# Optimization experiments

Measured on AMD Instinct MI355X. Metric: run time of the kernel, lower is better.

Reference implementation:

```python
import jax, jax.numpy as jnp
import numpy as np

H, KV, D, WIN = 16, 4, 128, 1024


def _rope(x, cos, sin):
    # x: [B, H, S, D]; cos/sin: [1, 1, S, D//2]
    d = x.shape[-1] // 2
    x1, x2 = x[..., :d], x[..., d:]
    S = x.shape[2]
    c, s = cos[:, :, :S], sin[:, :, :S]
    return jnp.concatenate([x1 * c + x2 * s, -x1 * s + x2 * c], axis=-1)


def _rms_norm(x):
    eps = jnp.finfo(x.dtype).eps
    return x * jax.lax.rsqrt(jnp.mean(jnp.square(x), axis=-1, keepdims=True) + eps)


def setup_inputs() -> dict:
    key = jax.random.key(0)
    ks = jax.random.split(key, 7)
    B, S, E = 2, 2048, 2048
    return {
        "x": jax.random.normal(ks[0], (B, S, E), jnp.float32),
        "cos": jax.random.normal(ks[1], (1, 1, S, D // 2), jnp.float32),
        "sin": jax.random.normal(ks[2], (1, 1, S, D // 2), jnp.float32),
        "Wq": jax.random.normal(ks[3], (H * D, E), jnp.float32) * 0.02,
        "Wk": jax.random.normal(ks[4], (KV * D, E), jnp.float32) * 0.02,
        "Wv": jax.random.normal(ks[5], (KV * D, E), jnp.float32) * 0.02,
        "Wo": jax.random.normal(ks[6], (E, H * D), jnp.float32) * 0.02,
    }


def reference(x, cos, sin, Wq, Wk, Wv, Wo):
    B, S, E = x.shape
    rep = H // KV
    # projections -> [B, heads, S, D]
    q = (x @ Wq.T).reshape(B, S, H, D).transpose(0, 2, 1, 3)
    k = (x @ Wk.T).reshape(B, S, KV, D).transpose(0, 2, 1, 3)
    v = (x @ Wv.T).reshape(B, S, KV, D).transpose(0, 2, 1, 3)
    # GQA: materialize repeated K/V heads (matches repeat_interleave)
    k = jnp.repeat(k, rep, axis=1)
    v = jnp.repeat(v, rep, axis=1)
    # RoPE then QK RMSNorm (no learned scale)
    q = _rms_norm(_rope(q, cos, sin))
    k = _rms_norm(_rope(k, cos, sin))
    scores = jnp.einsum("bhqd,bhkd->bhqk", q, k) * (D ** -0.5)
    # causal & sliding-window mask
    i = jnp.arange(S)[:, None]
    j = jnp.arange(S)[None, :]
    mask = (i >= j) & (jnp.abs(i - j) < WIN)
    scores = jnp.where(mask[None, None], scores, -jnp.inf)
    attn = jax.nn.softmax(scores, axis=-1)
    out = jnp.einsum("bhqk,bhkd->bhqd", attn, v)
    out = out.transpose(0, 2, 1, 3).reshape(B, S, H * D)
    return out @ Wo.T
```

## Files before the change

kernel.cpp:

```cpp
#include <hip/hip_runtime.h>
#include <stdint.h>

using bf16 = __bf16;
typedef __bf16 bf16x8 __attribute__((ext_vector_type(8)));
typedef __bf16 bf16x4 __attribute__((ext_vector_type(4)));
typedef float f32x4 __attribute__((ext_vector_type(4)));

#define H_ 16
#define KV_ 4
#define D_ 128
#define WIN_ 1024
#define B_ 2
#define S_ 2048
#define E_ 2048
#define HD_ 2048

__device__ __forceinline__ void gld_lds16(const void* gptr, void* lptr) {
    __builtin_amdgcn_global_load_lds(
        (__attribute__((address_space(1))) void*)(uintptr_t)gptr,
        (__attribute__((address_space(3))) void*)(uintptr_t)lptr, 16, 0, 0);
}

__global__ __launch_bounds__(256) void cvt_all(const float* __restrict__ x,
                                               const float* __restrict__ wq,
                                               const float* __restrict__ wk,
                                               const float* __restrict__ wv,
                                               const float* __restrict__ wo,
                                               bf16* __restrict__ dst) {
    int i = (blockIdx.x * 256 + threadIdx.x) * 4;
    const float* src;
    int off;
    if (i < 8388608)       { src = x;  off = 0; }
    else if (i < 12582912) { src = wq; off = 8388608; }
    else if (i < 13631488) { src = wk; off = 12582912; }
    else if (i < 14680064) { src = wv; off = 13631488; }
    else                   { src = wo; off = 14680064; }
    const float4 v = *(const float4*)(src + (i - off));
    bf16x4 o = {(bf16)v.x, (bf16)v.y, (bf16)v.z, (bf16)v.w};
    *(bf16x4*)(dst + i) = o;
}


template <typename OutT>
__global__ __launch_bounds__(256) void gemm_bt(const bf16* __restrict__ A,
                                               const bf16* __restrict__ W,
                                               OutT* __restrict__ C, int K, int ldc) {
    __shared__ alignas(16) bf16 As[128 * 64];
    __shared__ alignas(16) bf16 Bs[128 * 64];
    const int t = threadIdx.x;
    const int lane = t & 63;
    const int wave = t >> 6;
    const int l15 = lane & 15;
    const int quad = lane >> 4;
    const int fsw = l15 & 7;
    const int wm = (wave & 1) * 64;
    const int wn = (wave >> 1) * 64;
    const int m0 = blockIdx.x * 128;
    const int n0 = blockIdx.y * 128;

    f32x4 acc[4][4] = {};

    const int sr = t >> 3;
    const int su = ((t & 7) ^ ((t >> 3) & 7)) * 8;
    const bf16* Ap = A + (size_t)(m0 + sr) * K + su;
    const bf16* Wp = W + (size_t)(n0 + sr) * K + su;

    for (int k0 = 0; k0 < K; k0 += 64) {
#pragma unroll
        for (int c = 0; c < 4; ++c) {
            gld_lds16(Ap + k0 + (size_t)c * 32 * K, &As[c * 2048 + t * 8]);
            gld_lds16(Wp + k0 + (size_t)c * 32 * K, &Bs[c * 2048 + t * 8]);
        }
        __syncthreads();
#pragma unroll
        for (int kh = 0; kh < 2; ++kh) {
            bf16x8 af[4], bfr[4];
#pragma unroll
            for (int i = 0; i < 4; ++i) {
                af[i] = *(const bf16x8*)&As[(wm + i * 16 + l15) * 64 +
                                            (((kh * 4 + quad) ^ fsw) * 8)];
                bfr[i] = *(const bf16x8*)&Bs[(wn + i * 16 + l15) * 64 +
                                             (((kh * 4 + quad) ^ fsw) * 8)];
            }
#pragma unroll
            for (int i = 0; i < 4; ++i)
#pragma unroll
                for (int j = 0; j < 4; ++j)
                    acc[i][j] =
                        __builtin_amdgcn_mfma_f32_16x16x32_bf16(af[i], bfr[j], acc[i][j], 0, 0, 0);
        }
        __syncthreads();
    }
#pragma unroll
    for (int i = 0; i < 4; ++i) {
        const int row = m0 + wm + i * 16 + quad * 4;
#pragma unroll
        for (int j = 0; j < 4; ++j) {
            const int col = n0 + wn + j * 16 + l15;
#pragma unroll
            for (int r = 0; r < 4; ++r) C[(size_t)(row + r) * ldc + col] = (OutT)acc[i][j][r];
        }
    }
}

__global__ __launch_bounds__(256) void gemm_qkv_rope(const bf16* __restrict__ A,
                                                     const bf16* __restrict__ W,
                                                     const float* __restrict__ cosp,
                                                     const float* __restrict__ sinp,
                                                     bf16* __restrict__ qn,
                                                     bf16* __restrict__ kn,
                                                     bf16* __restrict__ vt) {
    __shared__ alignas(16) unsigned char smem[128 * 136 * 2];
    bf16* As = (bf16*)smem;
    bf16* Bs = (bf16*)(smem + 16384);
    bf16* Cs = (bf16*)smem;
    const int t = threadIdx.x;
    const int lane = t & 63;
    const int wave = t >> 6;
    const int l15 = lane & 15;
    const int quad = lane >> 4;
    const int fsw = l15 & 7;
    const int wm = (wave & 1) * 64;
    const int wn = (wave >> 1) * 64;
    const int m0 = blockIdx.x * 128;
    const int n0 = blockIdx.y * 128;
    const int K = E_;

    f32x4 acc[4][4] = {};

    const int sr = t >> 3;
    const int su = ((t & 7) ^ ((t >> 3) & 7)) * 8;
    const bf16* Ap = A + (size_t)(m0 + sr) * K + su;
    const bf16* Wp = W + (size_t)(n0 + sr) * K + su;

    for (int k0 = 0; k0 < K; k0 += 64) {
#pragma unroll
        for (int c = 0; c < 4; ++c) {
            gld_lds16(Ap + k0 + (size_t)c * 32 * K, &As[c * 2048 + t * 8]);
            gld_lds16(Wp + k0 + (size_t)c * 32 * K, &Bs[c * 2048 + t * 8]);
        }
        __syncthreads();
#pragma unroll
        for (int kh = 0; kh < 2; ++kh) {
            bf16x8 af[4], bfr[4];
#pragma unroll
            for (int i = 0; i < 4; ++i) {
                af[i] = *(const bf16x8*)&As[(wm + i * 16 + l15) * 64 +
                                            (((kh * 4 + quad) ^ fsw) * 8)];
                bfr[i] = *(const bf16x8*)&Bs[(wn + i * 16 + l15) * 64 +
                                             (((kh * 4 + quad) ^ fsw) * 8)];
            }
#pragma unroll
            for (int i = 0; i < 4; ++i)
#pragma unroll
                for (int j = 0; j < 4; ++j)
                    acc[i][j] =
                        __builtin_amdgcn_mfma_f32_16x16x32_bf16(af[i], bfr[j], acc[i][j], 0, 0, 0);
        }
        __syncthreads();
    }

#pragma unroll
    for (int i = 0; i < 4; ++i) {
        const int row = wm + i * 16 + quad * 4;
#pragma unroll
        for (int j = 0; j < 4; ++j) {
            const int col = wn + j * 16 + l15;
#pragma unroll
            for (int r = 0; r < 4; ++r) Cs[(row + r) * 136 + col] = (bf16)acc[i][j][r];
        }
    }
    __syncthreads();

    const int unit = n0 >> 7;
    if (unit < 20) {
        const int row = t >> 1;
        const int half = t & 1;
        const int gr = m0 + row;
        const int bb = gr >> 11;
        const int s = gr & 2047;
        const bf16* crow = &Cs[row * 136 + half * 32];
        const float* cp = cosp + s * 64 + half * 32;
        const float* sp = sinp + s * 64 + half * 32;
        bf16x8 xa[4], xb2[4];
#pragma unroll
        for (int u = 0; u < 4; ++u) {
            xa[u] = *(const bf16x8*)(crow + u * 8);
            xb2[u] = *(const bf16x8*)(crow + 64 + u * 8);
        }
        float y1[32], y2[32], ss = 0.0f;
#pragma unroll
        for (int u = 0; u < 4; ++u)
#pragma unroll
            for (int e = 0; e < 8; ++e) {
                const int jj = u * 8 + e;
                const float x1 = (float)xa[u][e];
                const float x2 = (float)xb2[u][e];
                const float c = cp[jj];
                const float sn = sp[jj];
                y1[jj] = x1 * c + x2 * sn;
                y2[jj] = x2 * c - x1 * sn;
                ss += y1[jj] * y1[jj] + y2[jj] * y2[jj];
            }
        ss += __shfl_xor(ss, 1, 64);
        float rr = rsqrtf(ss * (1.0f / 128.0f) + 1.1920929e-7f);
        bf16* dst;
        if (unit < 16) {
            rr *= 0.12751740f;
            dst = qn + ((size_t)(bb * H_ + unit) * S_ + s) * 128 + half * 32;
        } else {
            dst = kn + ((size_t)(bb * KV_ + (unit - 16)) * S_ + s) * 128 + half * 32;
        }
#pragma unroll
        for (int u = 0; u < 4; ++u) {
            bf16x8 p1, p2;
#pragma unroll
            for (int e = 0; e < 8; ++e) {
                p1[e] = (bf16)(y1[u * 8 + e] * rr);
                p2[e] = (bf16)(y2[u * 8 + e] * rr);
            }
            *(bf16x8*)(dst + u * 8) = p1;
            *(bf16x8*)(dst + 64 + u * 8) = p2;
        }
    } else {
        const int jv = unit - 20;
        const int d = t >> 1;
        const int sl0 = (t & 1) * 64;
        const int s0 = (m0 & 2047) + sl0;
        const int bb = m0 >> 11;
        bf16* vdst = vt + ((size_t)(bb * KV_ + jv) * 128 + d) * S_ + s0;
#pragma unroll
        for (int u = 0; u < 8; ++u) {
            bf16x8 pk;
#pragma unroll
            for (int e = 0; e < 8; ++e) pk[e] = Cs[(sl0 + u * 8 + e) * 136 + d];
            *(bf16x8*)(vdst + u * 8) = pk;
        }
    }
}

__global__ __launch_bounds__(256, 4) void attn_fwd(const bf16* __restrict__ Qn,
                                                   const bf16* __restrict__ Kn,
                                                   const bf16* __restrict__ Vt,
                                                   bf16* __restrict__ Out) {
    __shared__ alignas(16) bf16 Ks[64 * 128];
    __shared__ alignas(16) bf16 Vs[128 * 64];
    __shared__ alignas(16) bf16 Ps[4 * 16 * 64];

    const int t = threadIdx.x;
    const int lane = t & 63;
    const int wave = t >> 6;
    const int l15 = lane & 15;
    const int quad = lane >> 4;
    const int swz = l15 & 7;
    const int qb0 = blockIdx.x * 64;
    const int h = blockIdx.y;
    const int b = blockIdx.z;
    const int hk = h >> 2;
    const int qw0 = qb0 + wave * 16;

    const bf16* qbase = Qn + ((size_t)((b * H_ + h) * S_) + qw0 + l15) * 128;
    bf16x8 qf[4];
#pragma unroll
    for (int c4 = 0; c4 < 4; ++c4) qf[c4] = *(const bf16x8*)(qbase + c4 * 32 + quad * 8);

    f32x4 o[8] = {};
    float m = -1e30f, lsum = 0.0f;

    const bf16* kroot = Kn + (size_t)((b * KV_ + hk) * S_) * 128;
    const bf16* vroot = Vt + (size_t)((b * KV_ + hk) * 128) * S_;

    const int ku = (t & 15) ^ ((t >> 4) & 7);
    const int krow = t >> 4;
    const int vu = (t & 7) ^ ((t >> 3) & 7);
    const int vrow = t >> 3;
    const bf16* kst = kroot + (size_t)krow * 128 + ku * 8;
    const bf16* vst = vroot + (size_t)vrow * S_ + vu * 8;
    bf16* ksl = &Ks[t * 8];
    bf16* vsl = &Vs[t * 8];

    int lo = qb0 - (WIN_ - 1);
    if (lo < 0) lo = 0;
    const int kb_start = lo & ~63;
    const int kb_end = qb0 + 64;

    for (int kb = kb_start; kb < kb_end; kb += 64) {
#pragma unroll
        for (int c = 0; c < 4; ++c) gld_lds16(kst + (size_t)(kb + c * 16) * 128, ksl + c * 2048);
#pragma unroll
        for (int c = 0; c < 4; ++c) gld_lds16(vst + (size_t)(c * 32) * S_ + kb, vsl + c * 2048);
        __syncthreads();

        const bool wave_active = (kb + 63 >= qw0 - (WIN_ - 1));
        if (wave_active) {
            f32x4 sacc[4] = {};
#pragma unroll
            for (int kblk = 0; kblk < 4; ++kblk)
#pragma unroll
                for (int c4 = 0; c4 < 4; ++c4) {
                    bf16x8 kf = *(const bf16x8*)&Ks[(kblk * 16 + l15) * 128 +
                                                    (((c4 * 4 + quad) ^ swz) * 8)];
                    sacc[kblk] =
                        __builtin_amdgcn_mfma_f32_16x16x32_bf16(kf, qf[c4], sacc[kblk], 0, 0, 0);
                }

            const int q = qw0 + l15;
            float sv[16];
            const bool interior = (kb + 63 <= qw0) && (kb >= qw0 + 15 - (WIN_ - 1));
            if (interior) {
#pragma unroll
                for (int kblk = 0; kblk < 4; ++kblk)
#pragma unroll
                    for (int r = 0; r < 4; ++r) sv[kblk * 4 + r] = sacc[kblk][r];
            } else {
#pragma unroll
                for (int kblk = 0; kblk < 4; ++kblk)
#pragma unroll
                    for (int r = 0; r < 4; ++r) {
                        const int key = kb + kblk * 16 + quad * 4 + r;
                        const bool valid = (key <= q) && (q - key < WIN_);
                        sv[kblk * 4 + r] = valid ? sacc[kblk][r] : -1e30f;
                    }
            }
            float mc = sv[0];
#pragma unroll
            for (int i = 1; i < 16; ++i) mc = fmaxf(mc, sv[i]);
            mc = fmaxf(mc, __shfl_xor(mc, 16, 64));
            mc = fmaxf(mc, __shfl_xor(mc, 32, 64));
            const float mnew = fmaxf(m, mc);
            const float al = __builtin_amdgcn_exp2f(m - mnew);
            float ls = 0.0f;
#pragma unroll
            for (int i = 0; i < 16; ++i) {
                sv[i] = __builtin_amdgcn_exp2f(sv[i] - mnew);
                ls += sv[i];
            }
            ls += __shfl_xor(ls, 16, 64);
            ls += __shfl_xor(ls, 32, 64);
            lsum = lsum * al + ls;
            m = mnew;
#pragma unroll
            for (int dblk = 0; dblk < 8; ++dblk) o[dblk] *= al;

            bf16* pw = &Ps[wave * 1024 + l15 * 64];
#pragma unroll
            for (int kblk = 0; kblk < 4; ++kblk) {
                bf16x4 pb = {(bf16)sv[kblk * 4 + 0], (bf16)sv[kblk * 4 + 1],
                             (bf16)sv[kblk * 4 + 2], (bf16)sv[kblk * 4 + 3]};
                const int phys = (kblk * 2 + (quad >> 1)) ^ swz;
                *(bf16x4*)&pw[phys * 8 + (quad & 1) * 4] = pb;
            }
#pragma unroll
            for (int kc = 0; kc < 2; ++kc) {
                const int up = ((kc * 4 + quad) ^ swz) * 8;
                bf16x8 pfv = *(const bf16x8*)&pw[up];
#pragma unroll
                for (int dblk = 0; dblk < 8; ++dblk) {
                    bf16x8 vf = *(const bf16x8*)&Vs[(dblk * 16 + l15) * 64 + up];
                    o[dblk] = __builtin_amdgcn_mfma_f32_16x16x32_bf16(vf, pfv, o[dblk], 0, 0, 0);
                }
            }
        }
        __syncthreads();
    }

    const float inv = 1.0f / lsum;
    const int q = qw0 + l15;
    bf16* ob = Out + (size_t)(b * S_ + q) * HD_ + h * 128;
#pragma unroll
    for (int dblk = 0; dblk < 8; ++dblk) {
        bf16x4 ov = {(bf16)(o[dblk][0] * inv), (bf16)(o[dblk][1] * inv),
                     (bf16)(o[dblk][2] * inv), (bf16)(o[dblk][3] * inv)};
        *(bf16x4*)&ob[dblk * 16 + quad * 4] = ov;
    }
}

extern "C" void kernel_launch(void* const* d_in, const int* in_sizes, int n_in, void* d_out,
                              int out_size, void* d_ws, size_t ws_size, hipStream_t stream) {
    const float* x = (const float*)d_in[0];
    const float* cosp = (const float*)d_in[1];
    const float* sinp = (const float*)d_in[2];
    const float* Wq = (const float*)d_in[3];
    const float* Wk = (const float*)d_in[4];
    const float* Wv = (const float*)d_in[5];
    const float* Wo = (const float*)d_in[6];
    float* out = (float*)d_out;

    constexpr size_t MB = 1ull << 20;
    char* ws = (char*)d_ws;
    bf16* xb    = (bf16*)(ws + 0);
    bf16* wqkv  = (bf16*)(ws + 16 * MB);
    bf16* wo    = (bf16*)(ws + 28 * MB);
    bf16* qn    = (bf16*)(ws + 40 * MB);
    bf16* kn    = (bf16*)(ws + 56 * MB);
    bf16* vt    = (bf16*)(ws + 60 * MB);
    bf16* attnb = (bf16*)(ws + 64 * MB);

    cvt_all<<<18432, 256, 0, stream>>>(x, Wq, Wk, Wv, Wo, xb);
    gemm_qkv_rope<<<dim3(32, 24), 256, 0, stream>>>(xb, wqkv, cosp, sinp, qn, kn, vt);
    attn_fwd<<<dim3(32, 16, 2), 256, 0, stream>>>(qn, kn, vt, attnb);
    gemm_bt<float><<<dim3(32, 16), 256, 0, stream>>>(attnb, wo, out, 2048, 2048);
}
```

Before: 295.7 us.

## Process two 16-row query tiles per wave in attention with 128-thread blocks

The attention kernel now runs 2 waves per block instead of 4, and each wave handles 32 query rows as two 16-row sub-tiles sharing each K and V fragment read from LDS. K/V tile loads are split into 8 chunks per thread to suit the smaller block. This halves LDS fragment reads per MFMA and gives more independent MFMAs per wave. The cost is doubled accumulator register pressure, lower occupancy from the removed min-blocks bound, and fewer waves to hide the load barrier.

```diff
diff --git a/kernel.cpp b/kernel.cpp
--- a/kernel.cpp
+++ b/kernel.cpp
@@ -239,13 +239,13 @@
     }
 }
 
-__global__ __launch_bounds__(256, 4) void attn_fwd(const bf16* __restrict__ Qn,
-                                                   const bf16* __restrict__ Kn,
-                                                   const bf16* __restrict__ Vt,
-                                                   bf16* __restrict__ Out) {
+__global__ __launch_bounds__(128) void attn_fwd(const bf16* __restrict__ Qn,
+                                                const bf16* __restrict__ Kn,
+                                                const bf16* __restrict__ Vt,
+                                                bf16* __restrict__ Out) {
     __shared__ alignas(16) bf16 Ks[64 * 128];
     __shared__ alignas(16) bf16 Vs[128 * 64];
-    __shared__ alignas(16) bf16 Ps[4 * 16 * 64];
+    __shared__ alignas(16) bf16 Ps[2 * 16 * 64];
 
     const int t = threadIdx.x;
     const int lane = t & 63;
@@ -257,25 +257,25 @@
     const int h = blockIdx.y;
     const int b = blockIdx.z;
     const int hk = h >> 2;
-    const int qw0 = qb0 + wave * 16;
-
-    const bf16* qbase = Qn + ((size_t)((b * H_ + h) * S_) + qw0 + l15) * 128;
-    bf16x8 qf[4];
-#pragma unroll
-    for (int c4 = 0; c4 < 4; ++c4) qf[c4] = *(const bf16x8*)(qbase + c4 * 32 + quad * 8);
-
-    f32x4 o[8] = {};
-    float m = -1e30f, lsum = 0.0f;
+    const int qw0 = qb0 + wave * 32;
+
+    const bf16* qbaseA = Qn + ((size_t)((b * H_ + h) * S_) + qw0 + l15) * 128;
+    const bf16* qbaseB = qbaseA + 16 * 128;
+    bf16x8 qfA[4], qfB[4];
+#pragma unroll
+    for (int c4 = 0; c4 < 4; ++c4) {
+        qfA[c4] = *(const bf16x8*)(qbaseA + c4 * 32 + quad * 8);
+        qfB[c4] = *(const bf16x8*)(qbaseB + c4 * 32 + quad * 8);
+    }
+
+    f32x4 oA[8] = {}, oB[8] = {};
+    float mA = -1e30f, lA = 0.0f, mB = -1e30f, lB = 0.0f;
 
     const bf16* kroot = Kn + (size_t)((b * KV_ + hk) * S_) * 128;
     const bf16* vroot = Vt + (size_t)((b * KV_ + hk) * 128) * S_;
 
-    const int ku = (t & 15) ^ ((t >> 4) & 7);
-    const int krow = t >> 4;
-    const int vu = (t & 7) ^ ((t >> 3) & 7);
-    const int vrow = t >> 3;
-    const bf16* kst = kroot + (size_t)krow * 128 + ku * 8;
-    const bf16* vst = vroot + (size_t)vrow * S_ + vu * 8;
+    const bf16* kst = kroot + (size_t)(t >> 4) * 128 + ((t & 15) ^ (t >> 4)) * 8;
+    const bf16* vst = vroot + (size_t)(t >> 3) * S_ + ((t & 7) ^ ((t >> 3) & 7)) * 8;
     bf16* ksl = &Ks[t * 8];
     bf16* vsl = &Vs[t * 8];
 
@@ -284,94 +284,165 @@
     const int kb_start = lo & ~63;
     const int kb_end = qb0 + 64;
 
+    bf16* pw = &Ps[wave * 1024 + l15 * 64];
+
     for (int kb = kb_start; kb < kb_end; kb += 64) {
 #pragma unroll
-        for (int c = 0; c < 4; ++c) gld_lds16(kst + (size_t)(kb + c * 16) * 128, ksl + c * 2048);
-#pragma unroll
-        for (int c = 0; c < 4; ++c) gld_lds16(vst + (size_t)(c * 32) * S_ + kb, vsl + c * 2048);
+        for (int c = 0; c < 8; ++c) gld_lds16(kst + (size_t)(kb + c * 8) * 128, ksl + c * 1024);
+#pragma unroll
+        for (int c = 0; c < 8; ++c)
+            gld_lds16(vst + (size_t)(c * 16) * S_ + kb, vsl + c * 1024);
         __syncthreads();
 
         const bool wave_active = (kb + 63 >= qw0 - (WIN_ - 1));
         if (wave_active) {
-            f32x4 sacc[4] = {};
+            f32x4 sA[4] = {}, sB[4] = {};
 #pragma unroll
             for (int kblk = 0; kblk < 4; ++kblk)
 #pragma unroll
                 for (int c4 = 0; c4 < 4; ++c4) {
                     bf16x8 kf = *(const bf16x8*)&Ks[(kblk * 16 + l15) * 128 +
                                                     (((c4 * 4 + quad) ^ swz) * 8)];
-                    sacc[kblk] =
-                        __builtin_amdgcn_mfma_f32_16x16x32_bf16(kf, qf[c4], sacc[kblk], 0, 0, 0);
-                }
-
-            const int q = qw0 + l15;
-            float sv[16];
-            const bool interior = (kb + 63 <= qw0) && (kb >= qw0 + 15 - (WIN_ - 1));
-            if (interior) {
-#pragma unroll
-                for (int kblk = 0; kblk < 4; ++kblk)
-#pragma unroll
-                    for (int r = 0; r < 4; ++r) sv[kblk * 4 + r] = sacc[kblk][r];
-            } else {
-#pragma unroll
-                for (int kblk = 0; kblk < 4; ++kblk)
-#pragma unroll
-                    for (int r = 0; r < 4; ++r) {
-                        const int key = kb + kblk * 16 + quad * 4 + r;
-                        const bool valid = (key <= q) && (q - key < WIN_);
-                        sv[kblk * 4 + r] = valid ? sacc[kblk][r] : -1e30f;
-                    }
-            }
-            float mc = sv[0];
-#pragma unroll
-            for (int i = 1; i < 16; ++i) mc = fmaxf(mc, sv[i]);
-            mc = fmaxf(mc, __shfl_xor(mc, 16, 64));
-            mc = fmaxf(mc, __shfl_xor(mc, 32, 64));
-            const float mnew = fmaxf(m, mc);
-            const float al = __builtin_amdgcn_exp2f(m - mnew);
-            float ls = 0.0f;
-#pragma unroll
-            for (int i = 0; i < 16; ++i) {
-                sv[i] = __builtin_amdgcn_exp2f(sv[i] - mnew);
-                ls += sv[i];
-            }
-            ls += __shfl_xor(ls, 16, 64);
-            ls += __shfl_xor(ls, 32, 64);
-            lsum = lsum * al + ls;
-            m = mnew;
-#pragma unroll
-            for (int dblk = 0; dblk < 8; ++dblk) o[dblk] *= al;
-
-            bf16* pw = &Ps[wave * 1024 + l15 * 64];
-#pragma unroll
-            for (int kblk = 0; kblk < 4; ++kblk) {
-                bf16x4 pb = {(bf16)sv[kblk * 4 + 0], (bf16)sv[kblk * 4 + 1],
-                             (bf16)sv[kblk * 4 + 2], (bf16)sv[kblk * 4 + 3]};
-                const int phys = (kblk * 2 + (quad >> 1)) ^ swz;
-                *(bf16x4*)&pw[phys * 8 + (quad & 1) * 4] = pb;
+                    sA[kblk] = __builtin_amdgcn_mfma_f32_16x16x32_bf16(kf, qfA[c4], sA[kblk], 0, 0, 0);
+                    sB[kblk] = __builtin_amdgcn_mfma_f32_16x16x32_bf16(kf, qfB[c4], sB[kblk], 0, 0, 0);
+                }
+
+            bf16x8 pfA[2], pfB[2];
+
+            {
+                const int qg0 = qw0;
+                const int qq = qg0 + l15;
+                float sv[16];
+                const bool interior = (kb + 63 <= qg0) && (kb >= qg0 + 15 - (WIN_ - 1));
+                if (interior) {
+#pragma unroll
+                    for (int kblk = 0; kblk < 4; ++kblk)
+#pragma unroll
+                        for (int r = 0; r < 4; ++r) sv[kblk * 4 + r] = sA[kblk][r];
+                } else {
+#pragma unroll
+                    for (int kblk = 0; kblk < 4; ++kblk)
+#pragma unroll
+                        for (int r = 0; r < 4; ++r) {
+                            const int key = kb + kblk * 16 + quad * 4 + r;
+                            const bool valid = (key <= qq) && (qq - key < WIN_);
+                            sv[kblk * 4 + r] = valid ? sA[kblk][r] : -1e30f;
+                        }
+                }
+                float mc = sv[0];
+#pragma unroll
+                for (int i = 1; i < 16; ++i) mc = fmaxf(mc, sv[i]);
+                mc = fmaxf(mc, __shfl_xor(mc, 16, 64));
+                mc = fmaxf(mc, __shfl_xor(mc, 32, 64));
+                const float mnew = fmaxf(mA, mc);
+                const float al = __builtin_amdgcn_exp2f(mA - mnew);
+                float ls = 0.0f;
+#pragma unroll
+                for (int i = 0; i < 16; ++i) {
+                    sv[i] = __builtin_amdgcn_exp2f(sv[i] - mnew);
+                    ls += sv[i];
+                }
+                ls += __shfl_xor(ls, 16, 64);
+                ls += __shfl_xor(ls, 32, 64);
+                lA = lA * al + ls;
+                mA = mnew;
+#pragma unroll
+                for (int d = 0; d < 8; ++d) oA[d] *= al;
+#pragma unroll
+                for (int kblk = 0; kblk < 4; ++kblk) {
+                    bf16x4 pb = {(bf16)sv[kblk * 4 + 0], (bf16)sv[kblk * 4 + 1],
+                                 (bf16)sv[kblk * 4 + 2], (bf16)sv[kblk * 4 + 3]};
+                    const int phys = (kblk * 2 + (quad >> 1)) ^ swz;
+                    *(bf16x4*)&pw[phys * 8 + (quad & 1) * 4] = pb;
+                }
+                asm volatile("s_waitcnt lgkmcnt(0)" ::: "memory");
+                pfA[0] = *(const bf16x8*)&pw[((quad) ^ swz) * 8];
+                pfA[1] = *(const bf16x8*)&pw[((4 + quad) ^ swz) * 8];
+                asm volatile("s_waitcnt lgkmcnt(0)" ::: "memory");
+            }
+            {
+                const int qg0 = qw0 + 16;
+                const int qq = qg0 + l15;
+                float sv[16];
+                const bool interior = (kb + 63 <= qg0) && (kb >= qg0 + 15 - (WIN_ - 1));
+                if (interior) {
+#pragma unroll
+                    for (int kblk = 0; kblk < 4; ++kblk)
+#pragma unroll
+                        for (int r = 0; r < 4; ++r) sv[kblk * 4 + r] = sB[kblk][r];
+                } else {
+#pragma unroll
+                    for (int kblk = 0; kblk < 4; ++kblk)
+#pragma unroll
+                        for (int r = 0; r < 4; ++r) {
+                            const int key = kb + kblk * 16 + quad * 4 + r;
+                            const bool valid = (key <= qq) && (qq - key < WIN_);
+                            sv[kblk * 4 + r] = valid ? sB[kblk][r] : -1e30f;
+                        }
+                }
+                float mc = sv[0];
+#pragma unroll
+                for (int i = 1; i < 16; ++i) mc = fmaxf(mc, sv[i]);
+                mc = fmaxf(mc, __shfl_xor(mc, 16, 64));
+                mc = fmaxf(mc, __shfl_xor(mc, 32, 64));
+                const float mnew = fmaxf(mB, mc);
+                const float al = __builtin_amdgcn_exp2f(mB - mnew);
+                float ls = 0.0f;
+#pragma unroll
+                for (int i = 0; i < 16; ++i) {
+                    sv[i] = __builtin_amdgcn_exp2f(sv[i] - mnew);
+                    ls += sv[i];
+                }
+                ls += __shfl_xor(ls, 16, 64);
+                ls += __shfl_xor(ls, 32, 64);
+                lB = lB * al + ls;
+                mB = mnew;
+#pragma unroll
+                for (int d = 0; d < 8; ++d) oB[d] *= al;
+#pragma unroll
+                for (int kblk = 0; kblk < 4; ++kblk) {
+                    bf16x4 pb = {(bf16)sv[kblk * 4 + 0], (bf16)sv[kblk * 4 + 1],
+                                 (bf16)sv[kblk * 4 + 2], (bf16)sv[kblk * 4 + 3]};
+                    const int phys = (kblk * 2 + (quad >> 1)) ^ swz;
+                    *(bf16x4*)&pw[phys * 8 + (quad & 1) * 4] = pb;
+                }
+                asm volatile("s_waitcnt lgkmcnt(0)" ::: "memory");
+                pfB[0] = *(const bf16x8*)&pw[((quad) ^ swz) * 8];
+                pfB[1] = *(const bf16x8*)&pw[((4 + quad) ^ swz) * 8];
             }
 #pragma unroll
             for (int kc = 0; kc < 2; ++kc) {
                 const int up = ((kc * 4 + quad) ^ swz) * 8;
-                bf16x8 pfv = *(const bf16x8*)&pw[up];
 #pragma unroll
                 for (int dblk = 0; dblk < 8; ++dblk) {
                     bf16x8 vf = *(const bf16x8*)&Vs[(dblk * 16 + l15) * 64 + up];
-                    o[dblk] = __builtin_amdgcn_mfma_f32_16x16x32_bf16(vf, pfv, o[dblk], 0, 0, 0);
-                }
-            }
-        }
-        __syncthreads();
-    }
-
-    const float inv = 1.0f / lsum;
-    const int q = qw0 + l15;
-    bf16* ob = Out + (size_t)(b * S_ + q) * HD_ + h * 128;
-#pragma unroll
-    for (int dblk = 0; dblk < 8; ++dblk) {
-        bf16x4 ov = {(bf16)(o[dblk][0] * inv), (bf16)(o[dblk][1] * inv),
-                     (bf16)(o[dblk][2] * inv), (bf16)(o[dblk][3] * inv)};
-        *(bf16x4*)&ob[dblk * 16 + quad * 4] = ov;
+                    oA[dblk] = __builtin_amdgcn_mfma_f32_16x16x32_bf16(vf, pfA[kc], oA[dblk], 0, 0, 0);
+                    oB[dblk] = __builtin_amdgcn_mfma_f32_16x16x32_bf16(vf, pfB[kc], oB[dblk], 0, 0, 0);
+                }
+            }
+        }
+        __syncthreads();
+    }
+
+    {
+        const float inv = 1.0f / lA;
+        bf16* ob = Out + (size_t)(b * S_ + qw0 + l15) * HD_ + h * 128;
+#pragma unroll
+        for (int dblk = 0; dblk < 8; ++dblk) {
+            bf16x4 ov = {(bf16)(oA[dblk][0] * inv), (bf16)(oA[dblk][1] * inv),
+                         (bf16)(oA[dblk][2] * inv), (bf16)(oA[dblk][3] * inv)};
+            *(bf16x4*)&ob[dblk * 16 + quad * 4] = ov;
+        }
+    }
+    {
+        const float inv = 1.0f / lB;
+        bf16* ob = Out + (size_t)(b * S_ + qw0 + 16 + l15) * HD_ + h * 128;
+#pragma unroll
+        for (int dblk = 0; dblk < 8; ++dblk) {
+            bf16x4 ov = {(bf16)(oB[dblk][0] * inv), (bf16)(oB[dblk][1] * inv),
+                         (bf16)(oB[dblk][2] * inv), (bf16)(oB[dblk][3] * inv)};
+            *(bf16x4*)&ob[dblk * 16 + quad * 4] = ov;
+        }
     }
 }
 
@@ -398,6 +469,6 @@
 
     cvt_all<<<18432, 256, 0, stream>>>(x, Wq, Wk, Wv, Wo, xb);
     gemm_qkv_rope<<<dim3(32, 24), 256, 0, stream>>>(xb, wqkv, cosp, sinp, qn, kn, vt);
-    attn_fwd<<<dim3(32, 16, 2), 256, 0, stream>>>(qn, kn, vt, attnb);
+    attn_fwd<<<dim3(32, 16, 2), 128, 0, stream>>>(qn, kn, vt, attnb);
     gemm_bt<float><<<dim3(32, 16), 256, 0, stream>>>(attnb, wo, out, 2048, 2048);
 }
```

After: 319.8 us. 1.08x slower.
